# Kernel optimization log

Measured on AMD Instinct MI355X. Metric: run time of the kernel, lower is better.

## Reference

```python
import jax, jax.numpy as jnp
import numpy as np

BS = 4  # block_size == stride (non-overlapping)
EPS = 1e-5

def _to_blocks(x):
    # (B,C,H,W) -> (B*Hb*Wb, C, BS*BS), matching nn.Unfold(k=BS, stride=BS)
    B, C, H, W = x.shape
    Hb, Wb = H // BS, W // BS
    x = x.reshape(B, C, Hb, BS, Wb, BS).transpose(0, 2, 4, 1, 3, 5)
    return x.reshape(B * Hb * Wb, C, BS * BS)

def _from_blocks(x, B, C, H, W):
    Hb, Wb = H // BS, W // BS
    x = x.reshape(B, Hb, Wb, C, BS, BS).transpose(0, 3, 1, 4, 2, 5)
    return x.reshape(B, C, H, W)


def setup_inputs() -> dict:
    key = jax.random.key(0)
    ks = jax.random.split(key, 8)
    B, C, H, W = 8, 64, 256, 256
    P = 64  # proj_dim
    s = 1.0 / np.sqrt(C)
    return {
        "query_x": jax.random.normal(ks[0], (B, C, H, W), jnp.float32),
        "ref_x": jax.random.normal(ks[1], (B, C, H, W), jnp.float32),
        "Wq": jax.random.normal(ks[2], (P, C), jnp.float32) * s,
        "Wk": jax.random.normal(ks[3], (P, C), jnp.float32) * s,
        "Wv": jax.random.normal(ks[4], (P, C), jnp.float32) * s,
        "Wfc": jax.random.normal(ks[5], (C, P), jnp.float32) * (1.0 / np.sqrt(P)),
        "gn_w": jnp.ones((C,), jnp.float32),
        "gn_b": jnp.zeros((C,), jnp.float32),
    }


def reference(query_x, ref_x, Wq, Wk, Wv, Wfc, gn_w, gn_b):
    B, C, H, W = query_x.shape
    qb = _to_blocks(query_x)   # (Nb, C, 16)
    rb = _to_blocks(ref_x)     # (Nb, C, 16)

    q = jnp.einsum('pc,bcn->bpn', Wq, qb)
    k = jnp.einsum('pc,bcn->bpn', Wk, rb)
    v = jnp.einsum('pc,bcn->bpn', Wv, rb)

    energy = jnp.einsum('bcn,bcm->bnm', q, k)          # (Nb, 16, 16)
    attn = jax.nn.softmax(energy, axis=-1)
    out = jnp.einsum('bcm,bnm->bcn', v, attn)          # (Nb, P, 16)

    x = jnp.einsum('cp,bpn->bcn', Wfc, out)            # (Nb, C, 16)

    # GroupNorm(num_groups=1) over (C, N) per block
    mu = jnp.mean(x, axis=(1, 2), keepdims=True)
    var = jnp.var(x, axis=(1, 2), keepdims=True)
    x = (x - mu) * jax.lax.rsqrt(var + EPS)
    x = x * gn_w[None, :, None] + gn_b[None, :, None]

    x = x + qb  # residual
    return _from_blocks(x, B, C, H, W)
```

## Files before the change

### kernel.cpp

```cpp
#include <hip/hip_runtime.h>
#include <cstdint>


typedef float  f4    __attribute__((ext_vector_type(4)));
typedef float  f32x4 __attribute__((ext_vector_type(4)));
typedef short  s16x4 __attribute__((ext_vector_type(4)));
typedef short  s16x8 __attribute__((ext_vector_type(8)));
typedef unsigned short u16;
typedef __bf16 bf16;

#define MFMA16(a,b,c) __builtin_amdgcn_mfma_f32_16x16x16bf16_1k((a),(b),(c),0,0,0)
#define MFMA32(a,b,c) __builtin_amdgcn_mfma_f32_16x16x32_bf16((a),(b),(c),0,0,0)

__device__ __align__(16) u16 g_wpack[4 * 4096];

__device__ __forceinline__ u16 bfbits(float x) {
  return __builtin_bit_cast(u16, (bf16)x);
}

__device__ __forceinline__ void gload_lds16(const float* g, float* l) {
  __builtin_amdgcn_global_load_lds(
      (const __attribute__((address_space(1))) void*)g,
      (__attribute__((address_space(3))) void*)l, 16, 0, 0);
}

__global__ void prep_w(const float* __restrict__ Wq, const float* __restrict__ Wk,
                       const float* __restrict__ Wv, const float* __restrict__ Wfc)
{
  const int t = threadIdx.x;
  const float* Wm[3] = {Wq, Wk, Wv};
#pragma unroll
  for (int s = 0; s < 3; ++s) {
    const float* W = Wm[s];
    for (int e = t; e < 512; e += 256) {
      const int tile = e >> 6, l = e & 63;
      const int row = 16 * (tile >> 1) + (l & 15);
      const int col = 32 * (tile & 1) + 8 * (l >> 4);
#pragma unroll
      for (int j = 0; j < 8; ++j)
        g_wpack[s * 4096 + e * 8 + j] = bfbits(W[row * 64 + col + j]);
    }
  }
  for (int e = t; e < 1024; e += 256) {
    const int tile = e >> 6, l = e & 63;
    const int row = 16 * (tile >> 2) + (l & 15);
    const int col = 16 * (tile & 3) + 4 * (l >> 4);
#pragma unroll
    for (int j = 0; j < 4; ++j)
      g_wpack[3 * 4096 + e * 4 + j] = bfbits(Wfc[row * 64 + col + j]);
  }
}

__global__ void __launch_bounds__(256, 2)
cvbt9(const float* __restrict__ qx, const float* __restrict__ rx,
      const float* __restrict__ gw, const float* __restrict__ gb,
      float* __restrict__ out)
{
  __shared__ __align__(16) float sQ[2][4096];
  __shared__ __align__(16) float sR[4096];
  __shared__ u16   sP[4 * 320];
  __shared__ float sGn[128];

  const int tid  = threadIdx.x;
  const int wv   = tid >> 6, lane = tid & 63;
  const int n = lane & 15, g = lane >> 4, rp = n >> 2, wl = n & 3;

  if (tid < 128) sGn[tid] = (tid < 64) ? gw[tid] : gb[tid - 64];

  s16x8 Wq8[4][2], Wk8[4][2], Wv8[4][2];
  s16x4 Wf4[4][4];
#pragma unroll
  for (int a = 0; a < 4; ++a) {
#pragma unroll
    for (int c2 = 0; c2 < 2; ++c2) {
      Wq8[a][c2] = *(const s16x8*)(g_wpack + 0 * 4096 + ((a * 2 + c2) * 64 + lane) * 8);
      Wk8[a][c2] = *(const s16x8*)(g_wpack + 1 * 4096 + ((a * 2 + c2) * 64 + lane) * 8);
      Wv8[a][c2] = *(const s16x8*)(g_wpack + 2 * 4096 + ((a * 2 + c2) * 64 + lane) * 8);
    }
#pragma unroll
    for (int c4 = 0; c4 < 4; ++c4)
      Wf4[a][c4] = *(const s16x4*)(g_wpack + 3 * 4096 + ((a * 4 + c4) * 64 + lane) * 4);
  }

  uint32_t goff[4]; int lbase[4];
#pragma unroll
  for (int s = 0; s < 4; ++s) {
    const int j = s * 4 + wv;
    const int c = 4 * j + (lane >> 4);
    const int r = (lane >> 2) & 3, y = lane & 3;
    const int w4 = y ^ r ^ ((c >> 3) & 3);
    goff[s]  = (uint32_t)c * 65536u + (uint32_t)r * 256u + (uint32_t)w4 * 4u;
    lbase[s] = j * 256;
  }

  const int bid = blockIdx.x;
  const int wid = (bid & 7) * 96 + (bid >> 3);
  const int si0 = (wid < 512) ? wid * 11 : 5632 + (wid - 512) * 10;
  const int nt  = (wid < 512) ? 11 : 10;

  auto sbase = [](int si) -> uint32_t {
    return ((uint32_t)si >> 10) * 4194304u + (((uint32_t)si >> 4) & 63) * 1024u +
           ((uint32_t)si & 15) * 16u;
  };

  uint32_t sb = sbase(si0);
#pragma unroll
  for (int s = 0; s < 4; ++s) {
    gload_lds16(qx + sb + goff[s], &sQ[0][lbase[s]]);
    gload_lds16(rx + sb + goff[s], &sR[lbase[s]]);
  }
  asm volatile("s_waitcnt vmcnt(0) lgkmcnt(0)" ::: "memory");

  const f32x4 zero = {0.f, 0.f, 0.f, 0.f};
  u16* sPw = &sP[wv * 320];
  int pp = 0;

#pragma unroll 1
  for (int t = 0; t < nt; ++t) {
    const uint32_t nsb = sbase(si0 + t + 1);

    asm volatile("s_waitcnt vmcnt(4)" ::: "memory");
    __builtin_amdgcn_s_barrier();
    __builtin_amdgcn_sched_barrier(0);

    s16x8 frh[2], frl[2];
#pragma unroll
    for (int kt = 0; kt < 2; ++kt)
#pragma unroll
      for (int j = 0; j < 8; ++j) {
        const int addr = (32 * kt + 8 * g + j) * 64 + rp * 16 + 4 * (wv ^ rp ^ g) + wl;
        float x2 = sR[addr];
        bf16 h = (bf16)x2;
        frh[kt][j] = (short)__builtin_bit_cast(u16, h);
        frl[kt][j] = (short)bfbits(x2 - (float)h);
      }

    asm volatile("s_waitcnt lgkmcnt(0)" ::: "memory");
    __builtin_amdgcn_s_barrier();
    __builtin_amdgcn_sched_barrier(0);

    if (t + 1 < nt) {
#pragma unroll
      for (int s = 0; s < 4; ++s) {
        gload_lds16(qx + nsb + goff[s], &sQ[pp ^ 1][lbase[s]]);
        gload_lds16(rx + nsb + goff[s], &sR[lbase[s]]);
      }
    }
    __builtin_amdgcn_sched_barrier(0);

    f32x4 ak[4], av[4];
#pragma unroll
    for (int mt = 0; mt < 4; ++mt) { ak[mt] = zero; av[mt] = zero; }
#pragma unroll
    for (int mt = 0; mt < 4; ++mt)
#pragma unroll
      for (int kt = 0; kt < 2; ++kt) {
        ak[mt] = MFMA32(Wk8[mt][kt], frh[kt], ak[mt]);
        ak[mt] = MFMA32(Wk8[mt][kt], frl[kt], ak[mt]);
      }
#pragma unroll
    for (int nt2 = 0; nt2 < 4; ++nt2)
#pragma unroll
      for (int kt = 0; kt < 2; ++kt)
        av[nt2] = MFMA32(frh[kt], Wv8[nt2][kt], av[nt2]);

    s16x8 fqh[2], fql[2];
#pragma unroll
    for (int kt = 0; kt < 2; ++kt)
#pragma unroll
      for (int j = 0; j < 8; ++j) {
        const int addr = (32 * kt + 8 * g + j) * 64 + rp * 16 + 4 * (wv ^ rp ^ g) + wl;
        float x1 = sQ[pp][addr];
        bf16 h = (bf16)x1;
        fqh[kt][j] = (short)__builtin_bit_cast(u16, h);
        fql[kt][j] = (short)bfbits(x1 - (float)h);
      }
    f32x4 aq[4];
#pragma unroll
    for (int mt = 0; mt < 4; ++mt) {
      aq[mt] = zero;
#pragma unroll
      for (int kt = 0; kt < 2; ++kt) {
        aq[mt] = MFMA32(Wq8[mt][kt], fqh[kt], aq[mt]);
        aq[mt] = MFMA32(Wq8[mt][kt], fql[kt], aq[mt]);
      }
    }

    s16x4 qh[4], ql[4], kh[4], kl[4];
#pragma unroll
    for (int kt = 0; kt < 4; ++kt)
#pragma unroll
      for (int r = 0; r < 4; ++r) {
        bf16 h = (bf16)aq[kt][r];
        qh[kt][r] = (short)__builtin_bit_cast(u16, h);
        ql[kt][r] = (short)bfbits(aq[kt][r] - (float)h);
        bf16 h2 = (bf16)ak[kt][r];
        kh[kt][r] = (short)__builtin_bit_cast(u16, h2);
        kl[kt][r] = (short)bfbits(ak[kt][r] - (float)h2);
      }

    f32x4 e = zero;
#pragma unroll
    for (int kt = 0; kt < 4; ++kt) {
      e = MFMA16(qh[kt], kh[kt], e);
      e = MFMA16(qh[kt], kl[kt], e);
      e = MFMA16(ql[kt], kh[kt], e);
    }

#pragma unroll
    for (int r = 0; r < 4; ++r) {
      float x = e[r];
      float m = x;
      m = fmaxf(m, __shfl_xor(m, 1));
      m = fmaxf(m, __shfl_xor(m, 2));
      m = fmaxf(m, __shfl_xor(m, 4));
      m = fmaxf(m, __shfl_xor(m, 8));
      float p = __expf(x - m);
      float s = p;
      s += __shfl_xor(s, 1);
      s += __shfl_xor(s, 2);
      s += __shfl_xor(s, 4);
      s += __shfl_xor(s, 8);
      sPw[(4 * g + r) * 20 + n] = bfbits(p * __builtin_amdgcn_rcpf(s));
    }

    s16x4 pa = *(const s16x4*)&sPw[n * 20 + 4 * g];
    f32x4 ao[4];
#pragma unroll
    for (int mt = 0; mt < 4; ++mt) {
      s16x4 vb;
#pragma unroll
      for (int j = 0; j < 4; ++j) vb[j] = (short)bfbits(av[mt][j]);
      ao[mt] = MFMA16(vb, pa, zero);
    }

    s16x4 ob[4];
#pragma unroll
    for (int kt = 0; kt < 4; ++kt)
#pragma unroll
      for (int j = 0; j < 4; ++j) ob[kt][j] = (short)bfbits(ao[kt][j]);
    f32x4 xa[4];
#pragma unroll
    for (int mt = 0; mt < 4; ++mt) {
      xa[mt] = zero;
#pragma unroll
      for (int kt = 0; kt < 4; ++kt)
        xa[mt] = MFMA16(Wf4[mt][kt], ob[kt], xa[mt]);
    }

    float s1 = 0.f, s2 = 0.f;
#pragma unroll
    for (int mt = 0; mt < 4; ++mt)
#pragma unroll
      for (int r = 0; r < 4; ++r) {
        float v = xa[mt][r];
        s1 += v; s2 += v * v;
      }
#pragma unroll
    for (int mask = 1; mask < 64; mask <<= 1) {
      s1 += __shfl_xor(s1, mask);
      s2 += __shfl_xor(s2, mask);
    }
    const float mean = s1 * (1.f / 1024.f);
    const float var  = s2 * (1.f / 1024.f) - mean * mean;
    const float rstd = rsqrtf(var + 1e-5f);

#pragma unroll
    for (int mt = 0; mt < 4; ++mt)
#pragma unroll
      for (int r = 0; r < 4; ++r) {
        const int row = 16 * mt + 4 * g + r;
        const int addr = row * 64 + rp * 16 + 4 * (wv ^ rp ^ ((row >> 3) & 3)) + wl;
        sQ[pp][addr] = (xa[mt][r] - mean) * rstd * sGn[row] + sGn[64 + row] + sQ[pp][addr];
      }

    asm volatile("s_waitcnt lgkmcnt(0)" ::: "memory");
    __builtin_amdgcn_s_barrier();
    __builtin_amdgcn_sched_barrier(0);

#pragma unroll
    for (int s = 0; s < 4; ++s) {
      f4 o = *(const f4*)&sQ[pp][lbase[s] + lane * 4];
      __builtin_nontemporal_store(o, (f4*)(out + sb + goff[s]));
    }

    pp ^= 1;
    sb = nsb;
  }
}

extern "C" void kernel_launch(void* const* d_in, const int* in_sizes, int n_in,
                              void* d_out, int out_size, void* d_ws, size_t ws_size,
                              hipStream_t stream) {
  const float* qx  = (const float*)d_in[0];
  const float* rx  = (const float*)d_in[1];
  const float* Wq  = (const float*)d_in[2];
  const float* Wk  = (const float*)d_in[3];
  const float* Wv  = (const float*)d_in[4];
  const float* Wfc = (const float*)d_in[5];
  const float* gw  = (const float*)d_in[6];
  const float* gb  = (const float*)d_in[7];
  float* out = (float*)d_out;

  prep_w<<<dim3(1), dim3(256), 0, stream>>>(Wq, Wk, Wv, Wfc);
  cvbt9<<<dim3(768), dim3(256), 0, stream>>>(qx, rx, gw, gb, out);
}
```

Measured before the change: 115.9 us.

## Load ref tiles directly to registers and drop shared ref buffer

The ref_x tile is now read straight from global memory into registers, and its bf16 split plus the K/V MFMAs move after the Q projection so the load latency is hidden. The sR shared buffer and one barrier per iteration are removed, which cuts LDS traffic and footprint. The grid also grows from 768 to 1024 blocks with a uniform 8 tiles each, replacing the uneven 11/10 split. The risk is that the direct global reads use 4-byte scattered accesses with strides across channels, so coalescing may be worse than the 16-byte async LDS loads they replace.

```diff
diff --git a/kernel.cpp b/kernel.cpp
--- a/kernel.cpp
+++ b/kernel.cpp
@@ -52,12 +52,11 @@
 }
 
 __global__ void __launch_bounds__(256, 2)
-cvbt9(const float* __restrict__ qx, const float* __restrict__ rx,
-      const float* __restrict__ gw, const float* __restrict__ gb,
-      float* __restrict__ out)
+cvbt10(const float* __restrict__ qx, const float* __restrict__ rx,
+       const float* __restrict__ gw, const float* __restrict__ gb,
+       float* __restrict__ out)
 {
   __shared__ __align__(16) float sQ[2][4096];
-  __shared__ __align__(16) float sR[4096];
   __shared__ u16   sP[4 * 320];
   __shared__ float sGn[128];
 
@@ -94,21 +93,19 @@
   }
 
   const int bid = blockIdx.x;
-  const int wid = (bid & 7) * 96 + (bid >> 3);
-  const int si0 = (wid < 512) ? wid * 11 : 5632 + (wid - 512) * 10;
-  const int nt  = (wid < 512) ? 11 : 10;
+  const int wid = (bid & 7) * 128 + (bid >> 3);
+  const int si0 = wid * 8;
 
   auto sbase = [](int si) -> uint32_t {
     return ((uint32_t)si >> 10) * 4194304u + (((uint32_t)si >> 4) & 63) * 1024u +
            ((uint32_t)si & 15) * 16u;
   };
 
+  const uint32_t xro = (uint32_t)rp * 256u + (uint32_t)(4 * wv + wl);
+
   uint32_t sb = sbase(si0);
 #pragma unroll
-  for (int s = 0; s < 4; ++s) {
-    gload_lds16(qx + sb + goff[s], &sQ[0][lbase[s]]);
-    gload_lds16(rx + sb + goff[s], &sR[lbase[s]]);
-  }
+  for (int s = 0; s < 4; ++s) gload_lds16(qx + sb + goff[s], &sQ[0][lbase[s]]);
   asm volatile("s_waitcnt vmcnt(0) lgkmcnt(0)" ::: "memory");
 
   const f32x4 zero = {0.f, 0.f, 0.f, 0.f};
@@ -116,53 +113,27 @@
   int pp = 0;
 
 #pragma unroll 1
-  for (int t = 0; t < nt; ++t) {
+  for (int t = 0; t < 8; ++t) {
     const uint32_t nsb = sbase(si0 + t + 1);
 
     asm volatile("s_waitcnt vmcnt(4)" ::: "memory");
     __builtin_amdgcn_s_barrier();
     __builtin_amdgcn_sched_barrier(0);
 
-    s16x8 frh[2], frl[2];
+    float xr[2][8];
 #pragma unroll
     for (int kt = 0; kt < 2; ++kt)
 #pragma unroll
-      for (int j = 0; j < 8; ++j) {
-        const int addr = (32 * kt + 8 * g + j) * 64 + rp * 16 + 4 * (wv ^ rp ^ g) + wl;
-        float x2 = sR[addr];
-        bf16 h = (bf16)x2;
-        frh[kt][j] = (short)__builtin_bit_cast(u16, h);
-        frl[kt][j] = (short)bfbits(x2 - (float)h);
-      }
-
-    asm volatile("s_waitcnt lgkmcnt(0)" ::: "memory");
-    __builtin_amdgcn_s_barrier();
+      for (int j = 0; j < 8; ++j)
+        xr[kt][j] = rx[sb + xro + (uint32_t)(32 * kt + 8 * g + j) * 65536u];
     __builtin_amdgcn_sched_barrier(0);
 
-    if (t + 1 < nt) {
-#pragma unroll
-      for (int s = 0; s < 4; ++s) {
+    if (t < 7) {
+#pragma unroll
+      for (int s = 0; s < 4; ++s)
         gload_lds16(qx + nsb + goff[s], &sQ[pp ^ 1][lbase[s]]);
-        gload_lds16(rx + nsb + goff[s], &sR[lbase[s]]);
-      }
     }
     __builtin_amdgcn_sched_barrier(0);
-
-    f32x4 ak[4], av[4];
-#pragma unroll
-    for (int mt = 0; mt < 4; ++mt) { ak[mt] = zero; av[mt] = zero; }
-#pragma unroll
-    for (int mt = 0; mt < 4; ++mt)
-#pragma unroll
-      for (int kt = 0; kt < 2; ++kt) {
-        ak[mt] = MFMA32(Wk8[mt][kt], frh[kt], ak[mt]);
-        ak[mt] = MFMA32(Wk8[mt][kt], frl[kt], ak[mt]);
-      }
-#pragma unroll
-    for (int nt2 = 0; nt2 < 4; ++nt2)
-#pragma unroll
-      for (int kt = 0; kt < 2; ++kt)
-        av[nt2] = MFMA32(frh[kt], Wv8[nt2][kt], av[nt2]);
 
     s16x8 fqh[2], fql[2];
 #pragma unroll
@@ -185,6 +156,32 @@
         aq[mt] = MFMA32(Wq8[mt][kt], fql[kt], aq[mt]);
       }
     }
+
+    s16x8 frh[2], frl[2];
+#pragma unroll
+    for (int kt = 0; kt < 2; ++kt)
+#pragma unroll
+      for (int j = 0; j < 8; ++j) {
+        float x2 = xr[kt][j];
+        bf16 h = (bf16)x2;
+        frh[kt][j] = (short)__builtin_bit_cast(u16, h);
+        frl[kt][j] = (short)bfbits(x2 - (float)h);
+      }
+    f32x4 ak[4], av[4];
+#pragma unroll
+    for (int mt = 0; mt < 4; ++mt) { ak[mt] = zero; av[mt] = zero; }
+#pragma unroll
+    for (int mt = 0; mt < 4; ++mt)
+#pragma unroll
+      for (int kt = 0; kt < 2; ++kt) {
+        ak[mt] = MFMA32(Wk8[mt][kt], frh[kt], ak[mt]);
+        ak[mt] = MFMA32(Wk8[mt][kt], frl[kt], ak[mt]);
+      }
+#pragma unroll
+    for (int nt2 = 0; nt2 < 4; ++nt2)
+#pragma unroll
+      for (int kt = 0; kt < 2; ++kt)
+        av[nt2] = MFMA32(frh[kt], Wv8[nt2][kt], av[nt2]);
 
     s16x4 qh[4], ql[4], kh[4], kl[4];
 #pragma unroll
@@ -303,5 +300,5 @@
   float* out = (float*)d_out;
 
   prep_w<<<dim3(1), dim3(256), 0, stream>>>(Wq, Wk, Wv, Wfc);
-  cvbt9<<<dim3(768), dim3(256), 0, stream>>>(qx, rx, gw, gb, out);
-}
+  cvbt10<<<dim3(1024), dim3(256), 0, stream>>>(qx, rx, gw, gb, out);
+}
```

Result: faster. 109.2 us (-5.7%).
